# Optimization experiments

Hardware: AMD Instinct MI355X
Metric: run time of the kernel (lower is better)

The kernel has to match this reference:

```python
import jax, jax.numpy as jnp
import numpy as np
import math

B, S, D = 2, 1024, 2048
NH, NKV, HD = 16, 8, 128
NREP = NH // NKV
WINDOW = 256  # = max_seq_len; ReRoPE window


def _rope(x, cos, sin):
    # x: (b, s, h, d); cos/sin broadcastable to (b, s, h, d//2). Interleaved pairs (llama2.c style).
    b, s, h, d = x.shape
    xr, xi = x[..., ::2], x[..., 1::2]
    or_ = xr * cos - xi * sin
    oi = xr * sin + xi * cos
    return jnp.stack([or_, oi], axis=-1).reshape(b, s, h, d)


def setup_inputs() -> dict:
    key = jax.random.key(0)
    kx, kq, kk, kv, ko = jax.random.split(key, 5)
    # real RoPE tables (theta=10000), per-position, half head dim
    inv = 1.0 / (10000.0 ** (np.arange(0, HD, 2, dtype=np.float32) / HD))
    fr = np.outer(np.arange(S, dtype=np.float32), inv).astype(np.float32)  # (S, HD//2)
    sc = 0.02
    return {
        "x": jax.random.normal(kx, (B, S, D), jnp.float32),
        "freqs_cos": jnp.asarray(np.cos(fr)),
        "freqs_sin": jnp.asarray(np.sin(fr)),
        "wq": jax.random.normal(kq, (D, NH * HD), jnp.float32) * sc,
        "wk": jax.random.normal(kk, (D, NKV * HD), jnp.float32) * sc,
        "wv": jax.random.normal(kv, (D, NKV * HD), jnp.float32) * sc,
        "wo": jax.random.normal(ko, (NH * HD, D), jnp.float32) * sc,
    }


def reference(x, freqs_cos, freqs_sin, wq, wk, wv, wo):
    b, s, _ = x.shape
    xq = (x @ wq).reshape(b, s, NH, HD)
    xk = (x @ wk).reshape(b, s, NKV, HD)
    xv = (x @ wv).reshape(b, s, NKV, HD)

    cos = freqs_cos[:s][None, :, None, :]
    sin = freqs_sin[:s][None, :, None, :]
    q1 = _rope(xq, cos, sin)   # standard RoPE
    k1 = _rope(xk, cos, sin)

    # ReRoPE: queries rotated at the fixed clamp position = window; keys unrotated
    cw = freqs_cos[WINDOW][None, None, None, :]
    sw = freqs_sin[WINDOW][None, None, None, :]
    q2 = _rope(xq, cw, sw)
    k2 = xk

    rep = lambda a: jnp.repeat(a, NREP, axis=2)          # repeat_kv (GQA)
    heads = lambda a: a.transpose(0, 2, 1, 3)            # (b, h, s, d)
    q1, k1, v = heads(q1), heads(rep(k1)), heads(rep(xv))
    q2, k2 = heads(q2), heads(rep(k2))

    scale = 1.0 / math.sqrt(HD)
    s1 = jnp.einsum("bhqd,bhkd->bhqk", q1, k1) * scale
    s2 = jnp.einsum("bhqd,bhkd->bhqk", q2, k2) * scale

    i = jnp.arange(s)[:, None]
    j = jnp.arange(s)[None, :]
    causal = j <= i
    rect = causal & (j > i - WINDOW)                     # rectified_mask band
    scores = jnp.where(rect, s1, s2)
    scores = jnp.where(causal, scores, -jnp.inf)         # mask_inf (causal)

    attn = jax.nn.softmax(scores.astype(jnp.float32), axis=-1).astype(x.dtype)
    out = jnp.einsum("bhqk,bhkd->bhqd", attn, v)
    out = out.transpose(0, 2, 1, 3).reshape(b, s, NH * HD)
    return out @ wo
```

## Files before the change

### kernel.cpp

```cpp
#include <hip/hip_runtime.h>
#include <hip/hip_bf16.h>

#define BDIM 2
#define SDIM 1024
#define DDIM 2048
#define NH 16
#define NKV 8
#define HD 128
#define WINDOW 256

typedef __bf16 bf16;
typedef __bf16 bf16x4 __attribute__((ext_vector_type(4)));
typedef __bf16 bf16x8 __attribute__((ext_vector_type(8)));
typedef float f32x4 __attribute__((ext_vector_type(4)));

#define L2E 1.44269504088896341f

__device__ inline bf16x8 load8(const bf16* p) { return *reinterpret_cast<const bf16x8*>(p); }

__device__ __forceinline__ void gl_lds16(const bf16* g, bf16* l) {
  __builtin_amdgcn_global_load_lds(
      (__attribute__((address_space(1))) void*)g,
      (__attribute__((address_space(3))) void*)l,
      16, 0, 0);
}

__global__ __launch_bounds__(256) void prep(const float* __restrict__ x,
                                            const float* __restrict__ wq,
                                            const float* __restrict__ wk,
                                            const float* __restrict__ wv,
                                            const float* __restrict__ wo,
                                            bf16* __restrict__ xb,
                                            bf16* __restrict__ wqkvT,
                                            bf16* __restrict__ woT) {
  __shared__ bf16 tile[32][33];
  int z = blockIdx.z;
  int tx = threadIdx.x, ty = threadIdx.y;
  if (z == 4) {
    long i = (((long)blockIdx.y * 64 + blockIdx.x) * 256 + ty * 32 + tx) * 4;
    float4 a = *(const float4*)(x + i);
    bf16x4 o;
    o[0] = (bf16)a.x; o[1] = (bf16)a.y; o[2] = (bf16)a.z; o[3] = (bf16)a.w;
    *(bf16x4*)(xb + i) = o;
    return;
  }
  const float* src; bf16* dst; int C;
  if (z == 0)      { src = wq; dst = wqkvT;                 C = 2048; }
  else if (z == 1) { src = wk; dst = wqkvT + 2048L * 2048;  C = 1024; }
  else if (z == 2) { src = wv; dst = wqkvT + 3072L * 2048;  C = 1024; }
  else             { src = wo; dst = woT;                   C = 2048; }
  int c0 = blockIdx.x * 32, r0 = blockIdx.y * 32;
  if (c0 >= C) return;
  for (int yy = ty; yy < 32; yy += 8)
    tile[yy][tx] = (bf16)src[(long)(r0 + yy) * C + c0 + tx];
  __syncthreads();
  for (int yy = ty; yy < 32; yy += 8)
    dst[(long)(c0 + yy) * 2048 + r0 + tx] = tile[tx][yy];
}

#define BK 64
__global__ __launch_bounds__(256) void gemm_bt_n64(const bf16* __restrict__ A,
                                                   const bf16* __restrict__ Bt,
                                                   float* __restrict__ C,
                                                   int M, int N, int K) {
  __shared__ bf16 smem[2 * 12288];
  int t = threadIdx.x;
  int wid = t >> 6, lane = t & 63;
  int wm = (wid >> 1) * 64, wn = (wid & 1) * 32;
  int fm = lane & 15, quad = lane >> 4;

  int wg = blockIdx.y * 32 + blockIdx.x;
  int swz = (wg & 7) * 64 + (wg >> 3);
  int by = swz >> 5, bx = swz & 31;
  int m0 = by * 128, n0 = bx * 64;

  const bf16* Ag = A + (long)m0 * K;
  const bf16* Bg = Bt + (long)n0 * K;

  f32x4 acc[4][2] = {};

  auto stA = [&](bf16* dst, int k0, int p) {
    int idx = p * 256 + t;
    int row = idx >> 3, ccs = idx & 7;
    int gcol = ((ccs ^ (row & 7)) * 8);
    gl_lds16(&Ag[(long)row * K + k0 + gcol], &dst[idx * 8]);
  };
  auto stB = [&](bf16* dst, int k0, int p) {
    int idx = p * 256 + t;
    int row = idx >> 3, ccs = idx & 7;
    int gcol = ((ccs ^ (row & 7)) * 8);
    gl_lds16(&Bg[(long)row * K + k0 + gcol], &dst[idx * 8]);
  };
  auto cmp = [&](const bf16* As, const bf16* Bs, int ks) {
    int cc = (ks >> 3) + quad;
    bf16x8 af[4], bfr[2];
    for (int i = 0; i < 4; ++i) {
      int fr = wm + i * 16 + fm;
      af[i] = load8(&As[(fr * 8 + (cc ^ (fr & 7))) * 8]);
    }
    for (int j = 0; j < 2; ++j) {
      int fr = wn + j * 16 + fm;
      bfr[j] = load8(&Bs[(fr * 8 + (cc ^ (fr & 7))) * 8]);
    }
    __builtin_amdgcn_s_setprio(1);
    for (int i = 0; i < 4; ++i)
      for (int j = 0; j < 2; ++j)
        acc[i][j] = __builtin_amdgcn_mfma_f32_16x16x32_bf16(af[i], bfr[j], acc[i][j], 0, 0, 0);
    __builtin_amdgcn_s_setprio(0);
  };

  {
    bf16* As = smem; bf16* Bs = smem + 8192;
    stA(As, 0, 0); stA(As, 0, 1); stA(As, 0, 2); stA(As, 0, 3);
    stB(Bs, 0, 0); stB(Bs, 0, 1);
  }
  const int NT = K / BK;
  for (int kt = 0; kt < NT; ++kt) {
    int cur = kt & 1;
    bf16* As = smem + cur * 12288;
    bf16* Bs = As + 8192;
    if (kt + 1 < NT) {
      bf16* An = smem + (cur ^ 1) * 12288;
      bf16* Bn = An + 8192;
      int kn = (kt + 1) * BK;
      stA(An, kn, 0); stA(An, kn, 1); stB(Bn, kn, 0);
      asm volatile("s_waitcnt vmcnt(3)\n\ts_barrier" ::: "memory");
      cmp(As, Bs, 0);
      stA(An, kn, 2); stA(An, kn, 3); stB(Bn, kn, 1);
      cmp(As, Bs, 32);
      asm volatile("s_barrier" ::: "memory");
    } else {
      asm volatile("s_waitcnt vmcnt(0)\n\ts_barrier" ::: "memory");
      cmp(As, Bs, 0);
      cmp(As, Bs, 32);
    }
  }
  for (int i = 0; i < 4; ++i)
    for (int r = 0; r < 4; ++r) {
      int row = m0 + wm + i * 16 + quad * 4 + r;
      for (int j = 0; j < 2; ++j) {
        int col = n0 + wn + j * 16 + fm;
        C[(long)row * N + col] = acc[i][j][r];
      }
    }
}

#define VPITCH 130
__global__ __launch_bounds__(512) void gemm_qkv(const bf16* __restrict__ A,
                                                const bf16* __restrict__ Bt,
                                                const float* __restrict__ fc,
                                                const float* __restrict__ fs,
                                                bf16* __restrict__ q0,
                                                bf16* __restrict__ k1,
                                                bf16* __restrict__ k2,
                                                bf16* __restrict__ vT) {
  const int K = 2048;
  __shared__ bf16 smem[2 * 24576];
  int t = threadIdx.x;
  int wid = t >> 6, lane = t & 63;
  int wm = (wid >> 2) * 64, wn = (wid & 3) * 64;
  int fm = lane & 15, quad = lane >> 4;

  int wg = blockIdx.y * 16 + blockIdx.x;
  int swz = (wg & 7) * 32 + (wg >> 3);
  int by = swz >> 4, bx = swz & 15;
  int m0 = by * 128, n0 = bx * 256;

  const bf16* Ag = A + (long)m0 * K;
  const bf16* Bg = Bt + (long)n0 * K;

  f32x4 acc[4][4] = {};

  auto stA = [&](bf16* dst, int k0, int p) {
    int idx = p * 512 + t;
    int row = idx >> 3, ccs = idx & 7;
    int gcol = ((ccs ^ (row & 7)) * 8);
    gl_lds16(&Ag[(long)row * K + k0 + gcol], &dst[idx * 8]);
  };
  auto stB = [&](bf16* dst, int k0, int p) {
    int idx = p * 512 + t;
    int row = idx >> 3, ccs = idx & 7;
    int gcol = ((ccs ^ (row & 7)) * 8);
    gl_lds16(&Bg[(long)row * K + k0 + gcol], &dst[idx * 8]);
  };
  auto cmp = [&](const bf16* As, const bf16* Bs, int ks) {
    int cc = (ks >> 3) + quad;
    bf16x8 af[4], bfr[4];
    for (int i = 0; i < 4; ++i) {
      int fr = wm + i * 16 + fm;
      af[i] = load8(&As[(fr * 8 + (cc ^ (fr & 7))) * 8]);
    }
    for (int j = 0; j < 4; ++j) {
      int fr = wn + j * 16 + fm;
      bfr[j] = load8(&Bs[(fr * 8 + (cc ^ (fr & 7))) * 8]);
    }
    __builtin_amdgcn_s_setprio(1);
    for (int i = 0; i < 4; ++i)
      for (int j = 0; j < 4; ++j)
        acc[i][j] = __builtin_amdgcn_mfma_f32_16x16x32_bf16(af[i], bfr[j], acc[i][j], 0, 0, 0);
    __builtin_amdgcn_s_setprio(0);
  };

  {
    bf16* As = smem; bf16* Bs = smem + 8192;
    stA(As, 0, 0); stA(As, 0, 1);
    stB(Bs, 0, 0); stB(Bs, 0, 1); stB(Bs, 0, 2); stB(Bs, 0, 3);
  }
  const int NT = K / 64;
  for (int kt = 0; kt < NT; ++kt) {
    int cur = kt & 1;
    bf16* As = smem + cur * 24576;
    bf16* Bs = As + 8192;
    if (kt + 1 < NT) {
      bf16* An = smem + (cur ^ 1) * 24576;
      bf16* Bn = An + 8192;
      int kn = (kt + 1) * 64;
      stA(An, kn, 0); stA(An, kn, 1); stB(Bn, kn, 0);
      asm volatile("s_waitcnt vmcnt(3)\n\ts_barrier" ::: "memory");
      cmp(As, Bs, 0);
      stB(Bn, kn, 1); stB(Bn, kn, 2); stB(Bn, kn, 3);
      cmp(As, Bs, 32);
      asm volatile("s_barrier" ::: "memory");
    } else {
      asm volatile("s_waitcnt vmcnt(0)\n\ts_barrier" ::: "memory");
      cmp(As, Bs, 0);
      cmp(As, Bs, 32);
    }
  }

  if (n0 < 2048) {
    const float scale = 0.08838834764831845f;
    for (int i = 0; i < 4; ++i)
      for (int r = 0; r < 4; ++r) {
        int row = m0 + wm + i * 16 + quad * 4 + r;
        for (int j = 0; j < 4; ++j) {
          int gc = n0 + wn + j * 16 + fm;
          q0[(long)row * 2048 + gc] = (bf16)(acc[i][j][r] * scale);
        }
      }
  } else if (n0 < 3072) {
    float sgn = (lane & 1) ? 1.f : -1.f;
    float cwj[4], swj[4];
    for (int j = 0; j < 4; ++j) {
      int dp = ((wn + j * 16 + fm) & 127) >> 1;
      cwj[j] = fc[WINDOW * 64 + dp];
      swj[j] = fs[WINDOW * 64 + dp] * (-sgn);
    }
    for (int i = 0; i < 4; ++i)
      for (int r = 0; r < 4; ++r) {
        int row = m0 + wm + i * 16 + quad * 4 + r;
        int s = row & (SDIM - 1);
        for (int j = 0; j < 4; ++j) {
          int kc = n0 - 2048 + wn + j * 16 + fm;
          int dp = (kc & 127) >> 1;
          float v = acc[i][j][r];
          float pp = __shfl_xor(v, 1, 64);
          float c = fc[s * 64 + dp];
          float sn = fs[s * 64 + dp] * sgn;
          long dst = (long)row * 1024 + kc;
          k1[dst] = (bf16)(v * c + pp * sn);
          k2[dst] = (bf16)(v * cwj[j] + pp * swj[j]);
        }
      }
  } else {
    int vv0 = (n0 - 3072) >> 7;
    int s0l = m0 & (SDIM - 1);
    int bq = m0 >> 10;
    for (int half = 0; half < 2; ++half) {
      __syncthreads();
      if (((wn >> 7) & 1) == half) {
        for (int i = 0; i < 4; ++i)
          for (int j = 0; j < 4; ++j) {
            int col = (wn & 127) + j * 16 + fm;
            for (int r = 0; r < 4; ++r) {
              int rl = wm + i * 16 + quad * 4 + r;
              smem[col * VPITCH + rl] = (bf16)acc[i][j][r];
            }
          }
      }
      __syncthreads();
      bf16* vtg = vT + ((long)(bq * NKV + vv0 + half)) * 128 * 1024;
      for (int p = 0; p < 4; ++p) {
        int c = p * 512 + t;
        int d = c >> 4, sc = (c & 15) * 8;
        *(bf16x8*)&vtg[(long)d * 1024 + s0l + sc] = *(bf16x8*)&smem[d * VPITCH + sc];
      }
    }
  }
}

__global__ __launch_bounds__(256) void attn_kernel(const bf16* __restrict__ q0,
                                                   const bf16* __restrict__ k1,
                                                   const bf16* __restrict__ k2,
                                                   const bf16* __restrict__ vT,
                                                   const float* __restrict__ fc,
                                                   const float* __restrict__ fs,
                                                   bf16* __restrict__ aout) {
  __shared__ bf16 Ks[16384];
  __shared__ bf16 VTs[8192];
  __shared__ bf16 Pl[4][16][72];
  __shared__ float stats[4][16];

  int h = blockIdx.y;
  int b = blockIdx.z;
  int tile = b ? (15 - blockIdx.x) : blockIdx.x;
  int kv = h >> 1;
  int t = threadIdx.x;
  int w = t >> 6, lane = t & 63;
  int m = lane & 15, quad = lane >> 4;

  const bf16* k1g0 = k1 + ((long)b * SDIM) * 1024 + kv * 128;
  const bf16* k2g0 = k2 + ((long)b * SDIM) * 1024 + kv * 128;
  const bf16* vtg0 = vT + ((long)(b * NKV + kv)) * 128 * 1024;

  int t0 = tile * 64;
  int i0w = t0 + w * 16;

  const bf16* q0p = q0 + ((long)(b * SDIM + i0w + m)) * 2048 + h * 128 + quad * 8;
  bf16x8 q0f[4], q1f[4];
  int srow = i0w + m;
  for (int kc = 0; kc < 4; ++kc) {
    q0f[kc] = load8(q0p + kc * 32);
    for (int p4 = 0; p4 < 4; ++p4) {
      int dp = kc * 16 + quad * 4 + p4;
      float c = fc[srow * 64 + dp], sn = fs[srow * 64 + dp];
      float xr = (float)q0f[kc][2 * p4], xi = (float)q0f[kc][2 * p4 + 1];
      q1f[kc][2 * p4]     = (bf16)(xr * c - xi * sn);
      q1f[kc][2 * p4 + 1] = (bf16)(xr * sn + xi * c);
    }
  }

  f32x4 o[8] = {};
  float mrow = -INFINITY, lrow = 0.f;

  for (int j0 = 0; j0 < t0 + 64; j0 += 64) {
    bool c1 = (j0 + 63 > t0 - WINDOW);
    bool c2 = (j0 <= t0 + 63 - WINDOW);
    __syncthreads();
    for (int p = 0; p < 4; ++p) {
      int idx = p * 256 + t;
      int kr = idx >> 4, kcs = idx & 15;
      int kg = (kcs ^ (kr & 15)) * 8;
      if (c1) gl_lds16(&k1g0[(long)(j0 + kr) * 1024 + kg], &Ks[idx * 8]);
      if (c2) gl_lds16(&k2g0[(long)(j0 + kr) * 1024 + kg], &Ks[8192 + idx * 8]);
      int vd = idx >> 3, vcs = idx & 7;
      int vg = (vcs ^ (vd & 7)) * 8;
      gl_lds16(&vtg0[(long)vd * 1024 + j0 + vg], &VTs[idx * 8]);
    }
    __syncthreads();

    if (j0 < i0w + 16) {
      bool need1 = (j0 + 63 > i0w - WINDOW);
      bool need2 = (j0 <= i0w + 15 - WINDOW);
      f32x4 s1[4] = {}, s2[4] = {};
      if (need1)
        for (int st = 0; st < 4; ++st)
          for (int kc = 0; kc < 4; ++kc) {
            int cc = kc * 4 + quad;
            s1[st] = __builtin_amdgcn_mfma_f32_16x16x32_bf16(
                load8(&Ks[((st * 16 + m) * 16 + (cc ^ m)) * 8]), q1f[kc], s1[st], 0, 0, 0);
          }
      if (need2)
        for (int st = 0; st < 4; ++st)
          for (int kc = 0; kc < 4; ++kc) {
            int cc = kc * 4 + quad;
            s2[st] = __builtin_amdgcn_mfma_f32_16x16x32_bf16(
                load8(&Ks[8192 + ((st * 16 + m) * 16 + (cc ^ m)) * 8]), q0f[kc], s2[st], 0, 0, 0);
          }
      int i = i0w + m;
      float sv[4][4];
      for (int st = 0; st < 4; ++st)
        for (int r = 0; r < 4; ++r) {
          int j = j0 + st * 16 + quad * 4 + r;
          float v;
          if (j > i) v = -INFINITY;
          else if (j > i - WINDOW) v = s1[st][r];
          else v = s2[st][r];
          sv[st][r] = v;
        }
      float bm = -INFINITY;
      for (int st = 0; st < 4; ++st)
        for (int r = 0; r < 4; ++r) bm = fmaxf(bm, sv[st][r]);
      bm = fmaxf(bm, __shfl_xor(bm, 16, 64));
      bm = fmaxf(bm, __shfl_xor(bm, 32, 64));
      float mnew = fmaxf(mrow, bm);
      float alpha = exp2f((mrow - mnew) * L2E);
      float rs = 0.f;
      for (int st = 0; st < 4; ++st) {
        bf16x4 pk;
        for (int r = 0; r < 4; ++r) {
          float pvv = exp2f((sv[st][r] - mnew) * L2E);
          rs += pvv;
          pk[r] = (bf16)pvv;
        }
        *(bf16x4*)&Pl[w][m][st * 16 + quad * 4] = pk;
      }
      rs += __shfl_xor(rs, 16, 64);
      rs += __shfl_xor(rs, 32, 64);
      lrow = lrow * alpha + rs;
      mrow = mnew;
      if (lane < 16) stats[w][lane] = alpha;
      f32x4 av = *(f32x4*)&stats[w][quad * 4];
      for (int n8 = 0; n8 < 8; ++n8)
        for (int r = 0; r < 4; ++r) o[n8][r] *= av[r];
      for (int kc = 0; kc < 2; ++kc) {
        bf16x8 af = load8(&Pl[w][m][kc * 32 + quad * 8]);
        int cc = kc * 4 + quad;
        for (int n8 = 0; n8 < 8; ++n8) {
          int d = n8 * 16 + m;
          o[n8] = __builtin_amdgcn_mfma_f32_16x16x32_bf16(
              af, load8(&VTs[(d * 8 + (cc ^ (d & 7))) * 8]), o[n8], 0, 0, 0);
        }
      }
    }
  }

  if (lane < 16) stats[w][lane] = lrow;
  __builtin_amdgcn_s_waitcnt(0);
  f32x4 lv = *(f32x4*)&stats[w][quad * 4];
  for (int n8 = 0; n8 < 8; ++n8)
    for (int r = 0; r < 4; ++r) {
      int row = i0w + quad * 4 + r;
      float val = o[n8][r] / lv[r];
      aout[((long)(b * SDIM + row)) * 2048 + h * 128 + n8 * 16 + m] = (bf16)val;
    }
}

extern "C" void kernel_launch(void* const* d_in, const int* in_sizes, int n_in,
                              void* d_out, int out_size, void* d_ws, size_t ws_size,
                              hipStream_t stream) {
  const float* x  = (const float*)d_in[0];
  const float* fc = (const float*)d_in[1];
  const float* fs = (const float*)d_in[2];
  const float* wq = (const float*)d_in[3];
  const float* wk = (const float*)d_in[4];
  const float* wv = (const float*)d_in[5];
  const float* wo = (const float*)d_in[6];
  float* out = (float*)d_out;

  bf16* wqkvT = (bf16*)d_ws;
  bf16* woT   = wqkvT + 4096L * 2048;
  bf16* xb    = woT + 2048L * 2048;
  bf16* q0b   = xb + 2048L * 2048;
  bf16* k1b   = q0b + 2048L * 2048;
  bf16* k2b   = k1b + 2048L * 1024;
  bf16* vT    = k2b + 2048L * 1024;
  bf16* aout  = vT + 2048L * 1024;

  prep<<<dim3(64, 64, 5), dim3(32, 8), 0, stream>>>(x, wq, wk, wv, wo, xb, wqkvT, woT);

  gemm_qkv<<<dim3(16, 16), 512, 0, stream>>>(xb, wqkvT, fc, fs, q0b, k1b, k2b, vT);

  attn_kernel<<<dim3(16, 16, 2), 256, 0, stream>>>(q0b, k1b, k2b, vT, fc, fs, aout);

  gemm_bt_n64<<<dim3(32, 16), 256, 0, stream>>>(aout, woT, out, 2048, 2048, 2048);
}
```

Baseline: 226.0 us.

## Double-buffer K/V tiles and split attention into single-mode k1/k2 segments

Reorganizes the attention loop into a segment schedule. Fully-far tiles use the unrotated K with the original queries, and the windowed band uses rotated K. This way each segment does one QK MFMA pass instead of possibly two, and the V tile is shared per segment. K and V tiles are double-buffered in LDS with async global-to-LDS loads, using an explicit vmcnt wait plus barrier so the next tile's load overlaps compute. Masking is skipped for fully interior far segments, and the output rescale is skipped when no row max grows. The trade-off is a fixed vmcnt count tied to the number of loads per stage. The band segments may also re-load V tiles near the window boundary, since a j range can appear in both modes.

```diff
diff --git a/kernel.cpp b/kernel.cpp
--- a/kernel.cpp
+++ b/kernel.cpp
@@ -296,8 +296,8 @@
                                                    const float* __restrict__ fc,
                                                    const float* __restrict__ fs,
                                                    bf16* __restrict__ aout) {
-  __shared__ bf16 Ks[16384];
-  __shared__ bf16 VTs[8192];
+  __shared__ bf16 Kb[2][8192];
+  __shared__ bf16 Vb[2][8192];
   __shared__ bf16 Pl[4][16][72];
   __shared__ float stats[4][16];
 
@@ -330,89 +330,117 @@
     }
   }
 
-  f32x4 o[8] = {};
-  float mrow = -INFINITY, lrow = 0.f;
-
-  for (int j0 = 0; j0 < t0 + 64; j0 += 64) {
-    bool c1 = (j0 + 63 > t0 - WINDOW);
-    bool c2 = (j0 <= t0 + 63 - WINDOW);
-    __syncthreads();
+  int NS2 = tile >= 4 ? tile - 3 : 0;
+  int NSEG = NS2 + (tile < 4 ? tile + 1 : 5);
+  int j1base = tile >= 4 ? t0 - 256 : 0;
+
+  auto stage = [&](int s) {
+    int j0, md;
+    if (s < NS2) { j0 = s * 64; md = 2; } else { j0 = j1base + (s - NS2) * 64; md = 1; }
+    const bf16* kg0 = (md == 1) ? k1g0 : k2g0;
+    bf16* Kd = Kb[s & 1];
+    bf16* Vd = Vb[s & 1];
     for (int p = 0; p < 4; ++p) {
       int idx = p * 256 + t;
       int kr = idx >> 4, kcs = idx & 15;
       int kg = (kcs ^ (kr & 15)) * 8;
-      if (c1) gl_lds16(&k1g0[(long)(j0 + kr) * 1024 + kg], &Ks[idx * 8]);
-      if (c2) gl_lds16(&k2g0[(long)(j0 + kr) * 1024 + kg], &Ks[8192 + idx * 8]);
+      gl_lds16(&kg0[(long)(j0 + kr) * 1024 + kg], &Kd[idx * 8]);
       int vd = idx >> 3, vcs = idx & 7;
       int vg = (vcs ^ (vd & 7)) * 8;
-      gl_lds16(&vtg0[(long)vd * 1024 + j0 + vg], &VTs[idx * 8]);
-    }
-    __syncthreads();
-
-    if (j0 < i0w + 16) {
-      bool need1 = (j0 + 63 > i0w - WINDOW);
-      bool need2 = (j0 <= i0w + 15 - WINDOW);
-      f32x4 s1[4] = {}, s2[4] = {};
-      if (need1)
-        for (int st = 0; st < 4; ++st)
-          for (int kc = 0; kc < 4; ++kc) {
-            int cc = kc * 4 + quad;
-            s1[st] = __builtin_amdgcn_mfma_f32_16x16x32_bf16(
-                load8(&Ks[((st * 16 + m) * 16 + (cc ^ m)) * 8]), q1f[kc], s1[st], 0, 0, 0);
+      gl_lds16(&vtg0[(long)vd * 1024 + j0 + vg], &Vd[idx * 8]);
+    }
+  };
+
+  f32x4 o[8] = {};
+  float mrow = -INFINITY, lrow = 0.f;
+  int i = i0w + m;
+
+  stage(0);
+  for (int s = 0; s < NSEG; ++s) {
+    if (s + 1 < NSEG) {
+      stage(s + 1);
+      asm volatile("s_waitcnt vmcnt(8)\n\ts_barrier" ::: "memory");
+    } else {
+      asm volatile("s_waitcnt vmcnt(0)\n\ts_barrier" ::: "memory");
+    }
+    int j0, md;
+    if (s < NS2) { j0 = s * 64; md = 2; } else { j0 = j1base + (s - NS2) * 64; md = 1; }
+    bool fullseg = (md == 2) && (s < NS2 - 1);
+    const bf16* Ks = Kb[s & 1];
+    const bf16* VTs = Vb[s & 1];
+
+    f32x4 sc[4] = {};
+    if (md == 1) {
+      for (int st = 0; st < 4; ++st)
+        for (int kc = 0; kc < 4; ++kc) {
+          int cc = kc * 4 + quad;
+          sc[st] = __builtin_amdgcn_mfma_f32_16x16x32_bf16(
+              load8(&Ks[((st * 16 + m) * 16 + (cc ^ m)) * 8]), q1f[kc], sc[st], 0, 0, 0);
+        }
+    } else {
+      for (int st = 0; st < 4; ++st)
+        for (int kc = 0; kc < 4; ++kc) {
+          int cc = kc * 4 + quad;
+          sc[st] = __builtin_amdgcn_mfma_f32_16x16x32_bf16(
+              load8(&Ks[((st * 16 + m) * 16 + (cc ^ m)) * 8]), q0f[kc], sc[st], 0, 0, 0);
+        }
+    }
+
+    float sv[4][4];
+    for (int st = 0; st < 4; ++st)
+      for (int r = 0; r < 4; ++r) {
+        float v = sc[st][r];
+        if (!fullseg) {
+          int j = j0 + st * 16 + quad * 4 + r;
+          if (md == 1) {
+            if (j > i || j <= i - WINDOW) v = -INFINITY;
+          } else {
+            if (j > i - WINDOW) v = -INFINITY;
           }
-      if (need2)
-        for (int st = 0; st < 4; ++st)
-          for (int kc = 0; kc < 4; ++kc) {
-            int cc = kc * 4 + quad;
-            s2[st] = __builtin_amdgcn_mfma_f32_16x16x32_bf16(
-                load8(&Ks[8192 + ((st * 16 + m) * 16 + (cc ^ m)) * 8]), q0f[kc], s2[st], 0, 0, 0);
-          }
-      int i = i0w + m;
-      float sv[4][4];
-      for (int st = 0; st < 4; ++st)
-        for (int r = 0; r < 4; ++r) {
-          int j = j0 + st * 16 + quad * 4 + r;
-          float v;
-          if (j > i) v = -INFINITY;
-          else if (j > i - WINDOW) v = s1[st][r];
-          else v = s2[st][r];
-          sv[st][r] = v;
         }
-      float bm = -INFINITY;
-      for (int st = 0; st < 4; ++st)
-        for (int r = 0; r < 4; ++r) bm = fmaxf(bm, sv[st][r]);
-      bm = fmaxf(bm, __shfl_xor(bm, 16, 64));
-      bm = fmaxf(bm, __shfl_xor(bm, 32, 64));
-      float mnew = fmaxf(mrow, bm);
+        sv[st][r] = v;
+      }
+
+    float bm = -INFINITY;
+    for (int st = 0; st < 4; ++st)
+      for (int r = 0; r < 4; ++r) bm = fmaxf(bm, sv[st][r]);
+    bm = fmaxf(bm, __shfl_xor(bm, 16, 64));
+    bm = fmaxf(bm, __shfl_xor(bm, 32, 64));
+    float mnew = fmaxf(mrow, bm);
+    float rs = 0.f;
+    for (int st = 0; st < 4; ++st) {
+      bf16x4 pk;
+      for (int r = 0; r < 4; ++r) {
+        float pvv = exp2f((sv[st][r] - mnew) * L2E);
+        rs += pvv;
+        pk[r] = (bf16)pvv;
+      }
+      *(bf16x4*)&Pl[w][m][st * 16 + quad * 4] = pk;
+    }
+    rs += __shfl_xor(rs, 16, 64);
+    rs += __shfl_xor(rs, 32, 64);
+    if (__any(mnew > mrow)) {
       float alpha = exp2f((mrow - mnew) * L2E);
-      float rs = 0.f;
-      for (int st = 0; st < 4; ++st) {
-        bf16x4 pk;
-        for (int r = 0; r < 4; ++r) {
-          float pvv = exp2f((sv[st][r] - mnew) * L2E);
-          rs += pvv;
-          pk[r] = (bf16)pvv;
-        }
-        *(bf16x4*)&Pl[w][m][st * 16 + quad * 4] = pk;
-      }
-      rs += __shfl_xor(rs, 16, 64);
-      rs += __shfl_xor(rs, 32, 64);
       lrow = lrow * alpha + rs;
       mrow = mnew;
       if (lane < 16) stats[w][lane] = alpha;
       f32x4 av = *(f32x4*)&stats[w][quad * 4];
       for (int n8 = 0; n8 < 8; ++n8)
         for (int r = 0; r < 4; ++r) o[n8][r] *= av[r];
-      for (int kc = 0; kc < 2; ++kc) {
-        bf16x8 af = load8(&Pl[w][m][kc * 32 + quad * 8]);
-        int cc = kc * 4 + quad;
-        for (int n8 = 0; n8 < 8; ++n8) {
-          int d = n8 * 16 + m;
-          o[n8] = __builtin_amdgcn_mfma_f32_16x16x32_bf16(
-              af, load8(&VTs[(d * 8 + (cc ^ (d & 7))) * 8]), o[n8], 0, 0, 0);
-        }
-      }
-    }
+    } else {
+      lrow += rs;
+    }
+
+    for (int kc = 0; kc < 2; ++kc) {
+      bf16x8 af = load8(&Pl[w][m][kc * 32 + quad * 8]);
+      int cc = kc * 4 + quad;
+      for (int n8 = 0; n8 < 8; ++n8) {
+        int d = n8 * 16 + m;
+        o[n8] = __builtin_amdgcn_mfma_f32_16x16x32_bf16(
+            af, load8(&VTs[(d * 8 + (cc ^ (d & 7))) * 8]), o[n8], 0, 0, 0);
+      }
+    }
+    asm volatile("s_barrier" ::: "memory");
   }
 
   if (lane < 16) stats[w][lane] = lrow;
```

After: 228.8 us. No clear change (+1.3%).

## Read K/V straight from global memory per warp and split attention into far/window loops

Applied to the files above, without the earlier changes.

Drops the shared-memory K/V tiles and block-wide barriers, so each wavefront loads K and V fragments directly from global memory (relying on L2/L1). The key loop is split into a far region using unrotated keys and a window region using rotated keys, so each wave computes only one score MFMA set per block and masks instead of computing both. It skips the output rescale when no row max changes, and adds s_setprio around MFMA bursts. This removes sync and LDS staging overhead but risks uncoalesced, higher-latency global loads and redundant K/V traffic across the four waves.

```diff
diff --git a/kernel.cpp b/kernel.cpp
--- a/kernel.cpp
+++ b/kernel.cpp
@@ -296,8 +296,6 @@
                                                    const float* __restrict__ fc,
                                                    const float* __restrict__ fs,
                                                    bf16* __restrict__ aout) {
-  __shared__ bf16 Ks[16384];
-  __shared__ bf16 VTs[8192];
   __shared__ bf16 Pl[4][16][72];
   __shared__ float stats[4][16];
 
@@ -313,17 +311,16 @@
   const bf16* k2g0 = k2 + ((long)b * SDIM) * 1024 + kv * 128;
   const bf16* vtg0 = vT + ((long)(b * NKV + kv)) * 128 * 1024;
 
-  int t0 = tile * 64;
-  int i0w = t0 + w * 16;
+  int i0w = tile * 64 + w * 16;
+  int i = i0w + m;
 
   const bf16* q0p = q0 + ((long)(b * SDIM + i0w + m)) * 2048 + h * 128 + quad * 8;
   bf16x8 q0f[4], q1f[4];
-  int srow = i0w + m;
   for (int kc = 0; kc < 4; ++kc) {
     q0f[kc] = load8(q0p + kc * 32);
     for (int p4 = 0; p4 < 4; ++p4) {
       int dp = kc * 16 + quad * 4 + p4;
-      float c = fc[srow * 64 + dp], sn = fs[srow * 64 + dp];
+      float c = fc[i * 64 + dp], sn = fs[i * 64 + dp];
       float xr = (float)q0f[kc][2 * p4], xi = (float)q0f[kc][2 * p4 + 1];
       q1f[kc][2 * p4]     = (bf16)(xr * c - xi * sn);
       q1f[kc][2 * p4 + 1] = (bf16)(xr * sn + xi * c);
@@ -333,86 +330,92 @@
   f32x4 o[8] = {};
   float mrow = -INFINITY, lrow = 0.f;
 
-  for (int j0 = 0; j0 < t0 + 64; j0 += 64) {
-    bool c1 = (j0 + 63 > t0 - WINDOW);
-    bool c2 = (j0 <= t0 + 63 - WINDOW);
-    __syncthreads();
-    for (int p = 0; p < 4; ++p) {
-      int idx = p * 256 + t;
-      int kr = idx >> 4, kcs = idx & 15;
-      int kg = (kcs ^ (kr & 15)) * 8;
-      if (c1) gl_lds16(&k1g0[(long)(j0 + kr) * 1024 + kg], &Ks[idx * 8]);
-      if (c2) gl_lds16(&k2g0[(long)(j0 + kr) * 1024 + kg], &Ks[8192 + idx * 8]);
-      int vd = idx >> 3, vcs = idx & 7;
-      int vg = (vcs ^ (vd & 7)) * 8;
-      gl_lds16(&vtg0[(long)vd * 1024 + j0 + vg], &VTs[idx * 8]);
-    }
-    __syncthreads();
-
-    if (j0 < i0w + 16) {
-      bool need1 = (j0 + 63 > i0w - WINDOW);
-      bool need2 = (j0 <= i0w + 15 - WINDOW);
-      f32x4 s1[4] = {}, s2[4] = {};
-      if (need1)
-        for (int st = 0; st < 4; ++st)
-          for (int kc = 0; kc < 4; ++kc) {
-            int cc = kc * 4 + quad;
-            s1[st] = __builtin_amdgcn_mfma_f32_16x16x32_bf16(
-                load8(&Ks[((st * 16 + m) * 16 + (cc ^ m)) * 8]), q1f[kc], s1[st], 0, 0, 0);
-          }
-      if (need2)
-        for (int st = 0; st < 4; ++st)
-          for (int kc = 0; kc < 4; ++kc) {
-            int cc = kc * 4 + quad;
-            s2[st] = __builtin_amdgcn_mfma_f32_16x16x32_bf16(
-                load8(&Ks[8192 + ((st * 16 + m) * 16 + (cc ^ m)) * 8]), q0f[kc], s2[st], 0, 0, 0);
-          }
-      int i = i0w + m;
-      float sv[4][4];
-      for (int st = 0; st < 4; ++st)
-        for (int r = 0; r < 4; ++r) {
-          int j = j0 + st * 16 + quad * 4 + r;
-          float v;
-          if (j > i) v = -INFINITY;
-          else if (j > i - WINDOW) v = s1[st][r];
-          else v = s2[st][r];
-          sv[st][r] = v;
-        }
-      float bm = -INFINITY;
-      for (int st = 0; st < 4; ++st)
-        for (int r = 0; r < 4; ++r) bm = fmaxf(bm, sv[st][r]);
-      bm = fmaxf(bm, __shfl_xor(bm, 16, 64));
-      bm = fmaxf(bm, __shfl_xor(bm, 32, 64));
-      float mnew = fmaxf(mrow, bm);
+  auto smpv = [&](f32x4 (&sc)[4], int j0) {
+    float bm = -INFINITY;
+    for (int st = 0; st < 4; ++st)
+      for (int r = 0; r < 4; ++r) bm = fmaxf(bm, sc[st][r]);
+    bm = fmaxf(bm, __shfl_xor(bm, 16, 64));
+    bm = fmaxf(bm, __shfl_xor(bm, 32, 64));
+    float mnew = fmaxf(mrow, bm);
+    float rs = 0.f;
+    for (int st = 0; st < 4; ++st) {
+      bf16x4 pk;
+      for (int r = 0; r < 4; ++r) {
+        float pvv = exp2f((sc[st][r] - mnew) * L2E);
+        rs += pvv;
+        pk[r] = (bf16)pvv;
+      }
+      *(bf16x4*)&Pl[w][m][st * 16 + quad * 4] = pk;
+    }
+    rs += __shfl_xor(rs, 16, 64);
+    rs += __shfl_xor(rs, 32, 64);
+    if (__any(mnew > mrow)) {
       float alpha = exp2f((mrow - mnew) * L2E);
-      float rs = 0.f;
-      for (int st = 0; st < 4; ++st) {
-        bf16x4 pk;
-        for (int r = 0; r < 4; ++r) {
-          float pvv = exp2f((sv[st][r] - mnew) * L2E);
-          rs += pvv;
-          pk[r] = (bf16)pvv;
-        }
-        *(bf16x4*)&Pl[w][m][st * 16 + quad * 4] = pk;
-      }
-      rs += __shfl_xor(rs, 16, 64);
-      rs += __shfl_xor(rs, 32, 64);
       lrow = lrow * alpha + rs;
       mrow = mnew;
       if (lane < 16) stats[w][lane] = alpha;
       f32x4 av = *(f32x4*)&stats[w][quad * 4];
       for (int n8 = 0; n8 < 8; ++n8)
         for (int r = 0; r < 4; ++r) o[n8][r] *= av[r];
-      for (int kc = 0; kc < 2; ++kc) {
-        bf16x8 af = load8(&Pl[w][m][kc * 32 + quad * 8]);
+    } else {
+      lrow += rs;
+    }
+    for (int kc = 0; kc < 2; ++kc) {
+      bf16x8 af = load8(&Pl[w][m][kc * 32 + quad * 8]);
+      int cc = kc * 4 + quad;
+      __builtin_amdgcn_s_setprio(1);
+      for (int n8 = 0; n8 < 8; ++n8) {
+        int d = n8 * 16 + m;
+        o[n8] = __builtin_amdgcn_mfma_f32_16x16x32_bf16(
+            af, load8(&vtg0[(long)d * 1024 + j0 + cc * 8]), o[n8], 0, 0, 0);
+      }
+      __builtin_amdgcn_s_setprio(0);
+    }
+  };
+
+  int nf = (i0w + 15 - WINDOW >= 0) ? (((i0w + 15 - WINDOW) >> 6) + 1) : 0;
+  for (int jb = 0; jb < nf; ++jb) {
+    int j0 = jb << 6;
+    f32x4 sc[4] = {};
+    __builtin_amdgcn_s_setprio(1);
+    for (int st = 0; st < 4; ++st)
+      for (int kc = 0; kc < 4; ++kc) {
         int cc = kc * 4 + quad;
-        for (int n8 = 0; n8 < 8; ++n8) {
-          int d = n8 * 16 + m;
-          o[n8] = __builtin_amdgcn_mfma_f32_16x16x32_bf16(
-              af, load8(&VTs[(d * 8 + (cc ^ (d & 7))) * 8]), o[n8], 0, 0, 0);
+        sc[st] = __builtin_amdgcn_mfma_f32_16x16x32_bf16(
+            load8(&k2g0[(long)(j0 + st * 16 + m) * 1024 + cc * 8]), q0f[kc], sc[st], 0, 0, 0);
+      }
+    __builtin_amdgcn_s_setprio(0);
+    if (j0 + 63 > i0w - WINDOW) {
+      for (int st = 0; st < 4; ++st)
+        for (int r = 0; r < 4; ++r) {
+          int j = j0 + st * 16 + quad * 4 + r;
+          if (j > i - WINDOW) sc[st][r] = -INFINITY;
         }
-      }
-    }
+    }
+    smpv(sc, j0);
+  }
+
+  int wb0 = (i0w > 255) ? ((i0w - 255) >> 6) : 0;
+  int wend = (i0w >> 6) + 1;
+  for (int jb = wb0; jb < wend; ++jb) {
+    int j0 = jb << 6;
+    f32x4 sc[4] = {};
+    __builtin_amdgcn_s_setprio(1);
+    for (int st = 0; st < 4; ++st)
+      for (int kc = 0; kc < 4; ++kc) {
+        int cc = kc * 4 + quad;
+        sc[st] = __builtin_amdgcn_mfma_f32_16x16x32_bf16(
+            load8(&k1g0[(long)(j0 + st * 16 + m) * 1024 + cc * 8]), q1f[kc], sc[st], 0, 0, 0);
+      }
+    __builtin_amdgcn_s_setprio(0);
+    if ((j0 + 63 > i0w) || (j0 <= i0w + 15 - WINDOW)) {
+      for (int st = 0; st < 4; ++st)
+        for (int r = 0; r < 4; ++r) {
+          int j = j0 + st * 16 + quad * 4 + r;
+          if (j > i || j <= i - WINDOW) sc[st][r] = -INFINITY;
+        }
+    }
+    smpv(sc, j0);
   }
 
   if (lane < 16) stats[w][lane] = lrow;
```

Result: slower. 282.2 us (+24.9%).
